# Kernel tuning notes

Measured on AMD Instinct MI355X. Metric: run time of the kernel, lower is better.

## Reference

```python
import jax, jax.numpy as jnp
import numpy as np

N_NODES = 50000
N_EDGES = 800000
F_IN = 64
HID = 64
OUT = 2
N_GRAPHS = 500


def _lin_init(key, fan_in, fan_out):
    # uniform(-1/sqrt(fan_in), 1/sqrt(fan_in)), matching torch Linear default
    bound = 1.0 / np.sqrt(fan_in)
    return jax.random.uniform(key, (fan_in, fan_out), minval=-bound, maxval=bound, dtype=jnp.float32)


def setup_inputs() -> dict:
    key = jax.random.key(0)
    ks = jax.random.split(key, 16)
    x = jax.random.normal(ks[0], (N_NODES, F_IN), dtype=jnp.float32)
    edge_index = jax.random.randint(ks[1], (2, N_EDGES), 0, N_NODES, dtype=jnp.int64)
    batch = jnp.sort(jax.random.randint(ks[2], (N_NODES,), 0, N_GRAPHS, dtype=jnp.int64))
    dims = [(F_IN, HID), (HID, HID), (HID, HID)]
    params = {}
    for i, (fi, fo) in enumerate(dims, start=1):
        params[f"W{i}_rel"] = _lin_init(ks[2 + 3 * i], fi, fo)      # applied to aggregated neighbors
        params[f"W{i}_root"] = _lin_init(ks[3 + 3 * i], fi, fo)     # applied to self (no bias, PyG GraphConv)
        b_bound = 1.0 / np.sqrt(fi)
        params[f"b{i}"] = jax.random.uniform(ks[4 + 3 * i], (fo,), minval=-b_bound, maxval=b_bound, dtype=jnp.float32)
    params["Wf1"] = _lin_init(ks[13], HID, HID)
    params["bf1"] = jnp.zeros((HID,), dtype=jnp.float32)
    params["Wf2"] = _lin_init(ks[14], HID, OUT)
    params["bf2"] = jnp.zeros((OUT,), dtype=jnp.float32)
    return {"x": x, "edge_index": edge_index, "batch": batch, **params}


def _graph_conv(h, src, dst, W_rel, W_root, b):
    # PyG GraphConv: out_i = W_root h_i + W_rel * sum_{j->i} h_j + b
    agg = jax.ops.segment_sum(h[src], dst, num_segments=N_NODES)  # [N, F] gather + scatter-add
    return h @ W_root + agg @ W_rel + b


def reference(x, edge_index, batch,
              W1_rel, W1_root, b1,
              W2_rel, W2_root, b2,
              W3_rel, W3_root, b3,
              Wf1, bf1, Wf2, bf2):
    src, dst = edge_index[0], edge_index[1]
    # dropout is identity in eval mode
    h = jax.nn.relu(_graph_conv(x, src, dst, W1_rel, W1_root, b1))
    h = jax.nn.relu(_graph_conv(h, src, dst, W2_rel, W2_root, b2))
    h = jax.nn.relu(_graph_conv(h, src, dst, W3_rel, W3_root, b3))
    # global_mean_pool over graph ids
    sums = jax.ops.segment_sum(h, batch, num_segments=N_GRAPHS)            # [G, H]
    counts = jax.ops.segment_sum(jnp.ones((N_NODES,), h.dtype), batch, num_segments=N_GRAPHS)
    pooled = sums / jnp.maximum(counts, 1.0)[:, None]
    out = pooled @ Wf1 + bf1
    out = out @ Wf2 + bf2
    return out
```

## Files before the change

kernel.cpp:

```cpp
#include <hip/hip_runtime.h>


#define NFEAT 64
#define BCAP  6144

typedef unsigned short u16;
typedef unsigned int   u32;
typedef __attribute__((ext_vector_type(8))) short short8;
typedef __attribute__((ext_vector_type(4))) float f32x4;

__device__ __forceinline__ u16 f2bf(float f) {
    u32 u = __float_as_uint(f);
    u32 r = (u + 0x7fffu + ((u >> 16) & 1u)) >> 16;
    return (u16)r;
}
__device__ __forceinline__ float bflo(u32 u) { return __uint_as_float(u << 16); }
__device__ __forceinline__ float bfhi(u32 u) { return __uint_as_float(u & 0xffff0000u); }

#define CAST_BLKS 1600
__global__ __launch_bounds__(256) void prep(
    const float* __restrict__ x, u16* __restrict__ xb, int n8,
    const float* __restrict__ W1r, const float* __restrict__ W1l,
    const float* __restrict__ W2r, const float* __restrict__ W2l,
    const float* __restrict__ W3r, const float* __restrict__ W3l,
    u16* __restrict__ wimg, int* __restrict__ bcnt, int nbuck)
{
    const int bid = blockIdx.x;
    const int tid = threadIdx.x;

    if (bid < CAST_BLKS) {
        int i = bid * 256 + tid;
        if (i < n8) {
            const float4* p = (const float4*)(x + (size_t)i * 8);
            float4 a = p[0], b = p[1];
            uint4 o;
            o.x = f2bf(a.x) | ((u32)f2bf(a.y) << 16);
            o.y = f2bf(a.z) | ((u32)f2bf(a.w) << 16);
            o.z = f2bf(b.x) | ((u32)f2bf(b.y) << 16);
            o.w = f2bf(b.z) | ((u32)f2bf(b.w) << 16);
            *(uint4*)(xb + (size_t)i * 8) = o;
        }
    } else if (bid < CAST_BLKS + 6) {
        int m = bid - CAST_BLKS;
        int layer = m >> 1;
        int isrel = m & 1;
        const float* W = (m == 0) ? W1r : (m == 1) ? W1l :
                         (m == 2) ? W2r : (m == 3) ? W2l :
                         (m == 4) ? W3r : W3l;
        u16* img = wimg + (size_t)layer * (64 * 128);
        #pragma unroll
        for (int it = 0; it < 16; ++it) {
            int flat = it * 256 + tid;
            int k = flat >> 6, n = flat & 63;
            int ck = (k >> 3) + (isrel ? 8 : 0);
            int kin = k & 7;
            img[n * 128 + (((ck ^ (n & 7)) << 3) | kin)] = f2bf(W[k * 64 + n]);
        }
    } else {
        if (tid < nbuck) bcnt[tid] = 0;
    }
}

__global__ __launch_bounds__(256) void gemm_cat(
    const u16* __restrict__ hin, const u16* __restrict__ agg,
    const u16* __restrict__ wimg, const float* __restrict__ bias,
    u16* __restrict__ hout, int n_rows)
{
    __shared__ u16 als[64 * 128];
    __shared__ u16 wls[64 * 128];

    const int tid = threadIdx.x;
    const int row0 = blockIdx.x * 64;

    {
        const uint4* wsrc = (const uint4*)wimg;
        uint4* wdst = (uint4*)wls;
        #pragma unroll
        for (int it = 0; it < 4; ++it)
            wdst[it * 256 + tid] = wsrc[it * 256 + tid];
    }

    #pragma unroll
    for (int it = 0; it < 4; ++it) {
        int id = it * 256 + tid;
        int r = id >> 4, ch = id & 15;
        int gr = row0 + r;
        uint4 v = make_uint4(0, 0, 0, 0);
        if (gr < n_rows) {
            const u16* sp = (ch < 8) ? (hin + (size_t)gr * 64 + ch * 8)
                                     : (agg + (size_t)gr * 64 + (ch - 8) * 8);
            v = *(const uint4*)sp;
        }
        *(uint4*)&als[r * 128 + ((ch ^ (r & 7)) << 3)] = v;
    }
    __syncthreads();

    const int w = tid >> 6, l = tid & 63;
    const int l15 = l & 15;
    const int wrow0 = w * 16;

    short8 afr[4];
    #pragma unroll
    for (int ks = 0; ks < 4; ++ks) {
        int r = wrow0 + l15;
        int ck = ks * 4 + (l >> 4);
        afr[ks] = *(const short8*)&als[r * 128 + ((ck ^ (r & 7)) << 3)];
    }
    short8 bfr[4][4];
    #pragma unroll
    for (int nl = 0; nl < 4; ++nl)
        #pragma unroll
        for (int ks = 0; ks < 4; ++ks) {
            int cl = nl * 16 + l15;
            int ck = ks * 4 + (l >> 4);
            bfr[nl][ks] = *(const short8*)&wls[cl * 128 + ((ck ^ (cl & 7)) << 3)];
        }

    f32x4 acc[4];
    #pragma unroll
    for (int nl = 0; nl < 4; ++nl) {
        float bv = bias[nl * 16 + l15];
        f32x4 iv = {bv, bv, bv, bv};
        acc[nl] = iv;
    }
    #pragma unroll
    for (int nl = 0; nl < 4; ++nl)
        #pragma unroll
        for (int ks = 0; ks < 4; ++ks)
            acc[nl] = __builtin_amdgcn_mfma_f32_16x16x32_bf16(
                afr[ks], bfr[nl][ks], acc[nl], 0, 0, 0);

    const int rg = (l >> 4) * 4;
    #pragma unroll
    for (int reg = 0; reg < 4; ++reg) {
        int row = row0 + wrow0 + rg + reg;
        if (row < n_rows) {
            #pragma unroll
            for (int nl = 0; nl < 4; ++nl)
                hout[(size_t)row * 64 + nl * 16 + l15] =
                    f2bf(fmaxf(acc[nl][reg], 0.f));
        }
    }
}

__global__ __launch_bounds__(256) void part_bucket(
    const int* __restrict__ src, const int* __restrict__ dst, int ne,
    int* __restrict__ bcnt, u32* __restrict__ pairs)
{
    __shared__ int lcnt[256];
    __shared__ int lbase[256];
    const int t = threadIdx.x;
    const int e0 = blockIdx.x * 4096;

    lcnt[t] = 0;
    __syncthreads();

    int s_[16], d_[16];
    #pragma unroll
    for (int i = 0; i < 16; ++i) {
        int e = e0 + i * 256 + t;
        if (e < ne) { s_[i] = src[e]; d_[i] = dst[e]; }
        else        { s_[i] = 0;      d_[i] = -1; }
    }
    #pragma unroll
    for (int i = 0; i < 16; ++i)
        if (d_[i] >= 0) atomicAdd(&lcnt[d_[i] >> 8], 1);
    __syncthreads();

    {
        int c = lcnt[t];
        lbase[t] = (c > 0) ? atomicAdd(&bcnt[t], c) : 0;
    }
    __syncthreads();
    lcnt[t] = 0;
    __syncthreads();

    #pragma unroll
    for (int i = 0; i < 16; ++i)
        if (d_[i] >= 0) {
            int b = d_[i] >> 8;
            int o = atomicAdd(&lcnt[b], 1);
            pairs[(size_t)b * BCAP + lbase[b] + o] =
                (u32)s_[i] | ((u32)(d_[i] & 255) << 16);
        }
}

__global__ __launch_bounds__(64) void scan_offsets(const int* __restrict__ bcnt, int nbuck,
                                                   int* __restrict__ boff,
                                                   int* __restrict__ row_ptr, int nn) {
    const int t = threadIdx.x;
    int carry = 0;
    for (int base = 0; base < nbuck; base += 64) {
        int i = base + t;
        int v = (i < nbuck) ? bcnt[i] : 0;
        int inc = v;
        #pragma unroll
        for (int off = 1; off < 64; off <<= 1) {
            int x = __shfl_up(inc, off);
            if (t >= off) inc += x;
        }
        if (i < nbuck) boff[i] = carry + inc - v;
        carry += __shfl(inc, 63);
    }
    if (t == 0) row_ptr[nn] = carry;
}

__global__ __launch_bounds__(256) void build_csr(
    const u32* __restrict__ pairs, const int* __restrict__ bcnt,
    const int* __restrict__ boff, int nn,
    int* __restrict__ row_ptr, u16* __restrict__ csr_src)
{
    __shared__ u32 lp[BCAP];
    __shared__ int deg[256];
    __shared__ int tsum[256];
    __shared__ int lofs[256];
    __shared__ int cur[256];

    const int b = blockIdx.x;
    const int t = threadIdx.x;
    const int cnt   = bcnt[b];
    const int ebase = boff[b];
    const int n0    = b * 256;

    deg[t] = 0; cur[t] = 0;
    __syncthreads();

    for (int i = t; i < cnt; i += 256) {
        u32 p = pairs[(size_t)b * BCAP + i];
        lp[i] = p;
        atomicAdd(&deg[p >> 16], 1);
    }
    __syncthreads();

    tsum[t] = deg[t];
    __syncthreads();
    #pragma unroll
    for (int off = 1; off < 256; off <<= 1) {
        int x = (t >= off) ? tsum[t - off] : 0;
        __syncthreads();
        tsum[t] += x;
        __syncthreads();
    }
    int excl = (t > 0 ? tsum[t - 1] : 0);
    lofs[t] = ebase + excl;
    int node = n0 + t;
    if (node < nn) row_ptr[node] = ebase + excl;
    __syncthreads();

    for (int i = t; i < cnt; i += 256) {
        u32 p = lp[i];
        int dl = p >> 16;
        int pos = lofs[dl] + atomicAdd(&cur[dl], 1);
        csr_src[pos] = (u16)(p & 0xffffu);
    }
}

__global__ __launch_bounds__(256) void gather_agg(
    const u16* __restrict__ hb,
    const int* __restrict__ row_ptr,
    const u16* __restrict__ csr_src,
    u16* __restrict__ agg,
    int nn)
{
    const int node = blockIdx.x * 4 + (threadIdx.x >> 6);
    const int l = threadIdx.x & 63;
    if (node >= nn) return;
    const int s = row_ptr[node];
    const int e = row_ptr[node + 1];
    const int es = l >> 3;
    const int c  = l & 7;
    const uint4* hv = (const uint4*)hb;

    float a0=0.f,a1=0.f,a2=0.f,a3=0.f,a4=0.f,a5=0.f,a6=0.f,a7=0.f;
    for (int j = s; j < e; j += 16) {
        int je0 = j + es, je1 = j + es + 8;
        int jj0 = (je0 < e) ? je0 : (e - 1);
        int jj1 = (je1 < e) ? je1 : (e - 1);
        float m0 = (je0 < e) ? 1.f : 0.f;
        float m1 = (je1 < e) ? 1.f : 0.f;
        int s0 = csr_src[jj0];
        int s1 = csr_src[jj1];
        uint4 q0 = hv[(size_t)s0 * 8 + c];
        uint4 q1 = hv[(size_t)s1 * 8 + c];
        a0 = fmaf(m0, bflo(q0.x), a0);  a1 = fmaf(m0, bfhi(q0.x), a1);
        a2 = fmaf(m0, bflo(q0.y), a2);  a3 = fmaf(m0, bfhi(q0.y), a3);
        a4 = fmaf(m0, bflo(q0.z), a4);  a5 = fmaf(m0, bfhi(q0.z), a5);
        a6 = fmaf(m0, bflo(q0.w), a6);  a7 = fmaf(m0, bfhi(q0.w), a7);
        a0 = fmaf(m1, bflo(q1.x), a0);  a1 = fmaf(m1, bfhi(q1.x), a1);
        a2 = fmaf(m1, bflo(q1.y), a2);  a3 = fmaf(m1, bfhi(q1.y), a3);
        a4 = fmaf(m1, bflo(q1.z), a4);  a5 = fmaf(m1, bfhi(q1.z), a5);
        a6 = fmaf(m1, bflo(q1.w), a6);  a7 = fmaf(m1, bfhi(q1.w), a7);
    }
    #pragma unroll
    for (int msk = 8; msk <= 32; msk <<= 1) {
        a0 += __shfl_xor(a0, msk); a1 += __shfl_xor(a1, msk);
        a2 += __shfl_xor(a2, msk); a3 += __shfl_xor(a3, msk);
        a4 += __shfl_xor(a4, msk); a5 += __shfl_xor(a5, msk);
        a6 += __shfl_xor(a6, msk); a7 += __shfl_xor(a7, msk);
    }
    if (es == 0) {
        uint4 o;
        o.x = f2bf(a0) | ((u32)f2bf(a1) << 16);
        o.y = f2bf(a2) | ((u32)f2bf(a3) << 16);
        o.z = f2bf(a4) | ((u32)f2bf(a5) << 16);
        o.w = f2bf(a6) | ((u32)f2bf(a7) << 16);
        ((uint4*)agg)[(size_t)node * 8 + c] = o;
    }
}

__global__ __launch_bounds__(256) void pool_mlp(
    const u16* __restrict__ h,
    const int* __restrict__ batch,
    int n_nodes,
    const float* __restrict__ Wf1, const float* __restrict__ bf1,
    const float* __restrict__ Wf2, const float* __restrict__ bf2,
    float* __restrict__ out, int n_graphs)
{
    const int g = blockIdx.x;
    const int tid = threadIdx.x;

    int lo = 0, hi = n_nodes;
    while (lo < hi) { int mid = (lo + hi) >> 1; if (batch[mid] < g) lo = mid + 1; else hi = mid; }
    int s = lo;
    lo = s; hi = n_nodes;
    while (lo < hi) { int mid = (lo + hi) >> 1; if (batch[mid] < g + 1) lo = mid + 1; else hi = mid; }
    int e = lo;

    const int c16 = tid & 15;
    const int r16 = tid >> 4;
    const uint2* hv = (const uint2*)h;

    float4 acc = make_float4(0.f, 0.f, 0.f, 0.f);
    for (int i = s + r16; i < e; i += 16) {
        uint2 q = hv[(size_t)i * 16 + c16];
        acc.x += bflo(q.x); acc.y += bfhi(q.x);
        acc.z += bflo(q.y); acc.w += bfhi(q.y);
    }

    __shared__ float4 red[256];
    red[tid] = acc;
    __syncthreads();
    #pragma unroll
    for (int off = 8; off > 0; off >>= 1) {
        if (r16 < off) {
            float4 o = red[tid + off * 16];
            float4 m = red[tid];
            m.x += o.x; m.y += o.y; m.z += o.z; m.w += o.w;
            red[tid] = m;
        }
        __syncthreads();
    }

    __shared__ float pl[64];
    __shared__ float md[64];
    if (r16 == 0) {
        float inv = 1.0f / (float)((e - s) > 0 ? (e - s) : 1);
        float4 m = red[c16];
        pl[c16 * 4 + 0] = m.x * inv;
        pl[c16 * 4 + 1] = m.y * inv;
        pl[c16 * 4 + 2] = m.z * inv;
        pl[c16 * 4 + 3] = m.w * inv;
    }
    __syncthreads();

    if (tid < 64) {
        float m = bf1[tid];
        #pragma unroll 8
        for (int k = 0; k < 64; ++k)
            m += pl[k] * Wf1[k * 64 + tid];
        md[tid] = m;
    }
    __syncthreads();

    if (tid < 2) {
        float o = bf2[tid];
        #pragma unroll 8
        for (int k = 0; k < 64; ++k)
            o += md[k] * Wf2[k * 2 + tid];
        out[(size_t)g * 2 + tid] = o;
    }
}

extern "C" void kernel_launch(void* const* d_in, const int* in_sizes, int n_in,
                              void* d_out, int out_size, void* d_ws, size_t ws_size,
                              hipStream_t stream) {
    const float* x     = (const float*)d_in[0];
    const int*   ei    = (const int*)d_in[1];
    const int*   batch = (const int*)d_in[2];
    const float* W1_rel  = (const float*)d_in[3];
    const float* W1_root = (const float*)d_in[4];
    const float* b1      = (const float*)d_in[5];
    const float* W2_rel  = (const float*)d_in[6];
    const float* W2_root = (const float*)d_in[7];
    const float* b2      = (const float*)d_in[8];
    const float* W3_rel  = (const float*)d_in[9];
    const float* W3_root = (const float*)d_in[10];
    const float* b3      = (const float*)d_in[11];
    const float* Wf1     = (const float*)d_in[12];
    const float* bf1     = (const float*)d_in[13];
    const float* Wf2     = (const float*)d_in[14];
    const float* bf2     = (const float*)d_in[15];

    const int NN = in_sizes[0] / NFEAT;
    const int NE = in_sizes[1] / 2;
    const int NG = out_size / 2;

    const int* src = ei;
    const int* dst = ei + NE;

    const int nbuck = (NN + 255) / 256;

    u16*   hA      = (u16*)d_ws;
    u16*   hB      = hA + (size_t)NN * NFEAT;
    u16*   aggb    = hB + (size_t)NN * NFEAT;
    int*   row_ptr = (int*)(aggb + (size_t)NN * NFEAT);
    int*   bcnt    = row_ptr + (NN + 1);
    int*   boff    = bcnt + nbuck;
    u32*   pairs   = (u32*)(boff + nbuck);
    u16*   csr_src = (u16*)(pairs + (size_t)nbuck * BCAP);
    u16*   wimg    = csr_src + NE;

    const int gemm_grid = (NN + 63) / 64;
    const int node_grid = (NN + 3) / 4;
    const int part_grid = (NE + 4095) / 4096;
    const int n8        = NN * NFEAT / 8;

    prep<<<CAST_BLKS + 7, 256, 0, stream>>>(x, hB, n8,
        W1_root, W1_rel, W2_root, W2_rel, W3_root, W3_rel, wimg, bcnt, nbuck);

    part_bucket<<<part_grid, 256, 0, stream>>>(src, dst, NE, bcnt, pairs);
    scan_offsets<<<1, 64, 0, stream>>>(bcnt, nbuck, boff, row_ptr, NN);
    build_csr<<<nbuck, 256, 0, stream>>>(pairs, bcnt, boff, NN, row_ptr, csr_src);

    gather_agg<<<node_grid, 256, 0, stream>>>(hB, row_ptr, csr_src, aggb, NN);
    gemm_cat<<<gemm_grid, 256, 0, stream>>>(hB, aggb, wimg, b1, hA, NN);

    gather_agg<<<node_grid, 256, 0, stream>>>(hA, row_ptr, csr_src, aggb, NN);
    gemm_cat<<<gemm_grid, 256, 0, stream>>>(hA, aggb, wimg + 64 * 128, b2, hB, NN);

    gather_agg<<<node_grid, 256, 0, stream>>>(hB, row_ptr, csr_src, aggb, NN);
    gemm_cat<<<gemm_grid, 256, 0, stream>>>(hB, aggb, wimg + 2 * 64 * 128, b3, hA, NN);

    pool_mlp<<<NG, 256, 0, stream>>>(hA, batch, NN, Wf1, bf1, Wf2, bf2, (float*)d_out, NG);
}
```

Baseline: 124.6 us.

## Fuse global mean-pool sums into last GEMM epilogue via LDS and global atomics

The final GraphConv GEMM no longer writes the layer-3 node features. Its epilogue accumulates the ReLU outputs per graph into a shared-memory tile, then flushes nonzero partial sums to a float pooled buffer with atomics. The pool_mlp kernel becomes a 64-thread MLP head that only reads pooled sums and divides by the node count, and prep gains blocks that zero the pooled buffer. This removes the write and re-read of the final hidden state, at the cost of LDS and global atomic contention and nondeterministic float summation order.

```diff
diff --git a/kernel.cpp b/kernel.cpp
--- a/kernel.cpp
+++ b/kernel.cpp
@@ -23,7 +23,8 @@
     const float* __restrict__ W1r, const float* __restrict__ W1l,
     const float* __restrict__ W2r, const float* __restrict__ W2l,
     const float* __restrict__ W3r, const float* __restrict__ W3l,
-    u16* __restrict__ wimg, int* __restrict__ bcnt, int nbuck)
+    u16* __restrict__ wimg, int* __restrict__ bcnt, int nbuck,
+    float* __restrict__ pooled, int ng)
 {
     const int bid = blockIdx.x;
     const int tid = threadIdx.x;
@@ -56,15 +57,19 @@
             int kin = k & 7;
             img[n * 128 + (((ck ^ (n & 7)) << 3) | kin)] = f2bf(W[k * 64 + n]);
         }
+    } else if (bid == CAST_BLKS + 6) {
+        if (tid < nbuck) bcnt[tid] = 0;
     } else {
-        if (tid < nbuck) bcnt[tid] = 0;
+        int i = (bid - (CAST_BLKS + 7)) * 256 + tid;
+        if (i < ng * 16) ((float4*)pooled)[i] = make_float4(0.f, 0.f, 0.f, 0.f);
     }
 }
 
 __global__ __launch_bounds__(256) void gemm_cat(
     const u16* __restrict__ hin, const u16* __restrict__ agg,
     const u16* __restrict__ wimg, const float* __restrict__ bias,
-    u16* __restrict__ hout, int n_rows)
+    u16* __restrict__ hout, int n_rows,
+    int fuse_pool, const int* __restrict__ batch, float* __restrict__ pooled)
 {
     __shared__ u16 als[64 * 128];
     __shared__ u16 wls[64 * 128];
@@ -131,14 +136,52 @@
                 afr[ks], bfr[nl][ks], acc[nl], 0, 0, 0);
 
     const int rg = (l >> 4) * 4;
-    #pragma unroll
-    for (int reg = 0; reg < 4; ++reg) {
-        int row = row0 + wrow0 + rg + reg;
-        if (row < n_rows) {
-            #pragma unroll
-            for (int nl = 0; nl < 4; ++nl)
-                hout[(size_t)row * 64 + nl * 16 + l15] =
-                    f2bf(fmaxf(acc[nl][reg], 0.f));
+
+    if (!fuse_pool) {
+        #pragma unroll
+        for (int reg = 0; reg < 4; ++reg) {
+            int row = row0 + wrow0 + rg + reg;
+            if (row < n_rows) {
+                #pragma unroll
+                for (int nl = 0; nl < 4; ++nl)
+                    hout[(size_t)row * 64 + nl * 16 + l15] =
+                        f2bf(fmaxf(acc[nl][reg], 0.f));
+            }
+        }
+    } else {
+        float* pacc = (float*)als;
+        __syncthreads();
+        #pragma unroll
+        for (int it = 0; it < 4; ++it)
+            ((float4*)pacc)[it * 256 + tid] = make_float4(0.f, 0.f, 0.f, 0.f);
+        __syncthreads();
+
+        const int glo = batch[row0];
+        #pragma unroll
+        for (int reg = 0; reg < 4; ++reg) {
+            int row = row0 + wrow0 + rg + reg;
+            if (row < n_rows) {
+                int gi = batch[row] - glo;
+                #pragma unroll
+                for (int nl = 0; nl < 4; ++nl) {
+                    float v = fmaxf(acc[nl][reg], 0.f);
+                    int col = nl * 16 + l15;
+                    if (gi < 64) atomicAdd(&pacc[gi * 64 + col], v);
+                    else         unsafeAtomicAdd(&pooled[(size_t)(glo + gi) * 64 + col], v);
+                }
+            }
+        }
+        __syncthreads();
+
+        int last = row0 + 63; if (last > n_rows - 1) last = n_rows - 1;
+        int span = batch[last] - glo + 1;
+        if (span > 64) span = 64;
+        for (int i = tid; i < span * 64; i += 256) {
+            float v = pacc[i];
+            if (v != 0.f) {
+                int gi = i >> 6, col = i & 63;
+                unsafeAtomicAdd(&pooled[(size_t)(glo + gi) * 64 + col], v);
+            }
         }
     }
 }
@@ -308,16 +351,15 @@
     }
 }
 
-__global__ __launch_bounds__(256) void pool_mlp(
-    const u16* __restrict__ h,
-    const int* __restrict__ batch,
-    int n_nodes,
+__global__ __launch_bounds__(64) void mlp_head(
+    const float* __restrict__ pooled,
+    const int* __restrict__ batch, int n_nodes,
     const float* __restrict__ Wf1, const float* __restrict__ bf1,
     const float* __restrict__ Wf2, const float* __restrict__ bf2,
     float* __restrict__ out, int n_graphs)
 {
     const int g = blockIdx.x;
-    const int tid = threadIdx.x;
+    const int lane = threadIdx.x;
 
     int lo = 0, hi = n_nodes;
     while (lo < hi) { int mid = (lo + hi) >> 1; if (batch[mid] < g) lo = mid + 1; else hi = mid; }
@@ -326,58 +368,26 @@
     while (lo < hi) { int mid = (lo + hi) >> 1; if (batch[mid] < g + 1) lo = mid + 1; else hi = mid; }
     int e = lo;
 
-    const int c16 = tid & 15;
-    const int r16 = tid >> 4;
-    const uint2* hv = (const uint2*)h;
-
-    float4 acc = make_float4(0.f, 0.f, 0.f, 0.f);
-    for (int i = s + r16; i < e; i += 16) {
-        uint2 q = hv[(size_t)i * 16 + c16];
-        acc.x += bflo(q.x); acc.y += bfhi(q.x);
-        acc.z += bflo(q.y); acc.w += bfhi(q.y);
-    }
-
-    __shared__ float4 red[256];
-    red[tid] = acc;
-    __syncthreads();
-    #pragma unroll
-    for (int off = 8; off > 0; off >>= 1) {
-        if (r16 < off) {
-            float4 o = red[tid + off * 16];
-            float4 m = red[tid];
-            m.x += o.x; m.y += o.y; m.z += o.z; m.w += o.w;
-            red[tid] = m;
-        }
-        __syncthreads();
-    }
+    float inv = 1.0f / (float)((e - s) > 0 ? (e - s) : 1);
 
     __shared__ float pl[64];
     __shared__ float md[64];
-    if (r16 == 0) {
-        float inv = 1.0f / (float)((e - s) > 0 ? (e - s) : 1);
-        float4 m = red[c16];
-        pl[c16 * 4 + 0] = m.x * inv;
-        pl[c16 * 4 + 1] = m.y * inv;
-        pl[c16 * 4 + 2] = m.z * inv;
-        pl[c16 * 4 + 3] = m.w * inv;
-    }
-    __syncthreads();
-
-    if (tid < 64) {
-        float m = bf1[tid];
+    pl[lane] = pooled[(size_t)g * 64 + lane] * inv;
+    __syncthreads();
+
+    float m = bf1[lane];
+    #pragma unroll 8
+    for (int k = 0; k < 64; ++k)
+        m += pl[k] * Wf1[k * 64 + lane];
+    md[lane] = m;
+    __syncthreads();
+
+    if (lane < 2) {
+        float o = bf2[lane];
         #pragma unroll 8
         for (int k = 0; k < 64; ++k)
-            m += pl[k] * Wf1[k * 64 + tid];
-        md[tid] = m;
-    }
-    __syncthreads();
-
-    if (tid < 2) {
-        float o = bf2[tid];
-        #pragma unroll 8
-        for (int k = 0; k < 64; ++k)
-            o += md[k] * Wf2[k * 2 + tid];
-        out[(size_t)g * 2 + tid] = o;
+            o += md[k] * Wf2[k * 2 + lane];
+        out[(size_t)g * 2 + lane] = o;
     }
 }
 
@@ -419,27 +429,32 @@
     u32*   pairs   = (u32*)(boff + nbuck);
     u16*   csr_src = (u16*)(pairs + (size_t)nbuck * BCAP);
     u16*   wimg    = csr_src + NE;
+    float* pooled  = (float*)(wimg + 3 * 64 * 128);
 
     const int gemm_grid = (NN + 63) / 64;
     const int node_grid = (NN + 3) / 4;
     const int part_grid = (NE + 4095) / 4096;
     const int n8        = NN * NFEAT / 8;
-
-    prep<<<CAST_BLKS + 7, 256, 0, stream>>>(x, hB, n8,
-        W1_root, W1_rel, W2_root, W2_rel, W3_root, W3_rel, wimg, bcnt, nbuck);
+    const int pz_blocks = (NG * 16 + 255) / 256;
+
+    prep<<<CAST_BLKS + 7 + pz_blocks, 256, 0, stream>>>(x, hB, n8,
+        W1_root, W1_rel, W2_root, W2_rel, W3_root, W3_rel,
+        wimg, bcnt, nbuck, pooled, NG);
 
     part_bucket<<<part_grid, 256, 0, stream>>>(src, dst, NE, bcnt, pairs);
     scan_offsets<<<1, 64, 0, stream>>>(bcnt, nbuck, boff, row_ptr, NN);
     build_csr<<<nbuck, 256, 0, stream>>>(pairs, bcnt, boff, NN, row_ptr, csr_src);
 
     gather_agg<<<node_grid, 256, 0, stream>>>(hB, row_ptr, csr_src, aggb, NN);
-    gemm_cat<<<gemm_grid, 256, 0, stream>>>(hB, aggb, wimg, b1, hA, NN);
-
+    gemm_cat<<<gemm_grid, 256, 0, stream>>>(hB, aggb, wimg, b1, hA, NN,
+                                            0, batch, pooled);
     gather_agg<<<node_grid, 256, 0, stream>>>(hA, row_ptr, csr_src, aggb, NN);
-    gemm_cat<<<gemm_grid, 256, 0, stream>>>(hA, aggb, wimg + 64 * 128, b2, hB, NN);
-
+    gemm_cat<<<gemm_grid, 256, 0, stream>>>(hA, aggb, wimg + 64 * 128, b2, hB, NN,
+                                            0, batch, pooled);
     gather_agg<<<node_grid, 256, 0, stream>>>(hB, row_ptr, csr_src, aggb, NN);
-    gemm_cat<<<gemm_grid, 256, 0, stream>>>(hB, aggb, wimg + 2 * 64 * 128, b3, hA, NN);
-
-    pool_mlp<<<NG, 256, 0, stream>>>(hA, batch, NN, Wf1, bf1, Wf2, bf2, (float*)d_out, NG);
-}
+    gemm_cat<<<gemm_grid, 256, 0, stream>>>(hB, aggb, wimg + 2 * 64 * 128, b3, hA, NN,
+                                            1, batch, pooled);
+
+    mlp_head<<<NG, 64, 0, stream>>>(pooled, batch, NN, Wf1, bf1, Wf2, bf2,
+                                    (float*)d_out, NG);
+}
```

Measured after the change: 142.5 us. 1.14x slower.
